# Performance work log

Hardware: AMD Instinct MI355X
Metric: run time of the kernel (lower is better)

Reference implementation:

```python
import jax, jax.numpy as jnp
import numpy as np

N_EMBED = 1024
HEAD_SIZE = 128

def setup_inputs() -> dict:
    key = jax.random.key(0)
    k1, k2, k3, k4 = jax.random.split(key, 4)
    x = jax.random.normal(k1, (8, 2048, N_EMBED), dtype=jnp.float32)
    # torch.nn.Linear default init: U(-1/sqrt(in), 1/sqrt(in)); stored as [out, in],
    # we store transposed [in, out] for x @ W.
    bound = 1.0 / np.sqrt(N_EMBED)
    Wk = jax.random.uniform(k2, (N_EMBED, HEAD_SIZE), jnp.float32, -bound, bound)
    Wq = jax.random.uniform(k3, (N_EMBED, HEAD_SIZE), jnp.float32, -bound, bound)
    Wv = jax.random.uniform(k4, (N_EMBED, HEAD_SIZE), jnp.float32, -bound, bound)
    return {"x": x, "Wk": Wk, "Wq": Wq, "Wv": Wv}

def reference(x, Wk, Wq, Wv):
    # x: [B, T, E]
    k = jnp.einsum('bte,eh->bth', x, Wk)  # [B, T, H]
    q = jnp.einsum('bte,eh->bth', x, Wq)
    v = jnp.einsum('bte,eh->bth', x, Wv)
    scale = 1.0 / np.sqrt(HEAD_SIZE).astype(np.float32)
    wei = jnp.einsum('bqh,bkh->bqk', q, k) * scale  # [B, T, T]
    wei = jax.nn.softmax(wei, axis=-1)
    out = jnp.einsum('bqk,bkh->bqh', wei, v)  # [B, T, H]
    return out
```

## Files before the change

kernel.cpp:

```cpp
#include <hip/hip_runtime.h>

#define BATCH 8
#define TLEN 2048
#define EMB 1024
#define HDIM 128
#define SCALE 0.08838834764831845f
#define NSPLIT 4

typedef _Float16 f16x8 __attribute__((ext_vector_type(8)));
typedef _Float16 f16x4 __attribute__((ext_vector_type(4)));
typedef float f32x4 __attribute__((ext_vector_type(4)));

static __device__ __forceinline__ f32x4 mfma16(f16x8 a, f16x8 b, f32x4 c) {
    return __builtin_amdgcn_mfma_f32_16x16x32_f16(a, b, c, 0, 0, 0);
}

__global__ void prep_w(const float* __restrict__ Wk, const float* __restrict__ Wq,
                       const float* __restrict__ Wv, _Float16* __restrict__ wtf) {
    int g = blockIdx.x * 256 + threadIdx.x;
    int lane = g & 63;
    int kstep = (g >> 6) & 31;
    int ntile = g >> 11;
    int n = ntile * 16 + (lane & 15);
    int sel = n >> 7;
    int h = n & 127;
    const float* W = (sel == 0) ? Wk : (sel == 1) ? Wq : Wv;
    int kbase = kstep * 32 + (lane >> 4) * 8;
    f16x8 o;
#pragma unroll
    for (int j = 0; j < 8; j++) {
        float v = W[(size_t)(kbase + j) * HDIM + h];
        if (sel == 1) v *= SCALE;
        o[j] = (_Float16)v;
    }
    *(f16x8*)&wtf[(size_t)g * 8] = o;
}

__global__ __launch_bounds__(256, 2) void proj_kernel(
        const float* __restrict__ x, const _Float16* __restrict__ wtf,
        _Float16* __restrict__ kb, _Float16* __restrict__ qb, _Float16* __restrict__ vbT) {
    __shared__ _Float16 xs[2][32 * 72];
    const int t = threadIdx.x;
    const int m0 = blockIdx.x * 32;
    const int wv = t >> 6;
    const int lane = t & 63;
    const int m16 = lane & 15;
    const int quad = lane >> 4;
    const int n0 = wv * 96;
    const int r0 = t >> 4;
    const int c0 = (t & 15) * 4;

    const f32x4 zero4 = {0.f, 0.f, 0.f, 0.f};
    f32x4 acc[2][6];
#pragma unroll
    for (int mt = 0; mt < 2; mt++)
#pragma unroll
        for (int nt = 0; nt < 6; nt++) acc[mt][nt] = zero4;

    const float* xrow0 = &x[(size_t)(m0 + r0) * EMB + c0];
    const float* xrow1 = &x[(size_t)(m0 + 16 + r0) * EMB + c0];

    float4 xv[2][2];
    f16x8 bf[2][12];
    xv[0][0] = *(const float4*)(xrow0);
    xv[0][1] = *(const float4*)(xrow1);
#pragma unroll
    for (int ks = 0; ks < 2; ks++)
#pragma unroll
        for (int nt = 0; nt < 6; nt++)
            bf[0][ks * 6 + nt] = *(const f16x8*)
                &wtf[((size_t)((wv * 6 + nt) * 32 + ks) * 64 + lane) * 8];

#pragma unroll
    for (int it = 0; it < 16; it++) {
        const int cur = it & 1, nxt = cur ^ 1;
#pragma unroll
        for (int i = 0; i < 2; i++) {
            f16x4 h;
            h[0] = (_Float16)xv[cur][i].x; h[1] = (_Float16)xv[cur][i].y;
            h[2] = (_Float16)xv[cur][i].z; h[3] = (_Float16)xv[cur][i].w;
            *(f16x4*)&xs[cur][(r0 + 16 * i) * 72 + c0] = h;
        }
        __syncthreads();
        if (it < 15) {
            xv[nxt][0] = *(const float4*)(xrow0 + (it + 1) * 64);
            xv[nxt][1] = *(const float4*)(xrow1 + (it + 1) * 64);
#pragma unroll
            for (int ks = 0; ks < 2; ks++)
#pragma unroll
                for (int nt = 0; nt < 6; nt++)
                    bf[nxt][ks * 6 + nt] = *(const f16x8*)
                        &wtf[((size_t)((wv * 6 + nt) * 32 + (it + 1) * 2 + ks) * 64 + lane) * 8];
        }
#pragma unroll
        for (int ks = 0; ks < 2; ks++) {
            f16x8 a0 = *(const f16x8*)&xs[cur][m16 * 72 + ks * 32 + quad * 8];
            f16x8 a1 = *(const f16x8*)&xs[cur][(16 + m16) * 72 + ks * 32 + quad * 8];
#pragma unroll
            for (int nt = 0; nt < 6; nt++) {
                acc[0][nt] = mfma16(a0, bf[cur][ks * 6 + nt], acc[0][nt]);
                acc[1][nt] = mfma16(a1, bf[cur][ks * 6 + nt], acc[1][nt]);
            }
        }
    }
#pragma unroll
    for (int nt = 0; nt < 6; nt++) {
        int n = n0 + nt * 16 + m16;
        int nsel = n >> 7;
        int h = n & 127;
        if (nsel < 2) {
            _Float16* dst = (nsel == 0) ? kb : qb;
#pragma unroll
            for (int mt = 0; mt < 2; mt++)
#pragma unroll
                for (int r = 0; r < 4; r++) {
                    int mg = m0 + mt * 16 + quad * 4 + r;
                    dst[(size_t)mg * HDIM + h] = (_Float16)acc[mt][nt][r];
                }
        } else {
#pragma unroll
            for (int mt = 0; mt < 2; mt++) {
                int mg = m0 + mt * 16 + quad * 4;
                int bb = mg >> 11, tok = mg & 2047;
                f16x4 pk;
#pragma unroll
                for (int r = 0; r < 4; r++) pk[r] = (_Float16)acc[mt][nt][r];
                *(f16x4*)&vbT[((size_t)bb * HDIM + h) * TLEN + tok] = pk;
            }
        }
    }
}

__global__ __launch_bounds__(256, 3) void attn_kernel(
        const _Float16* __restrict__ qb, const _Float16* __restrict__ kb,
        const _Float16* __restrict__ vbT,
        _Float16* __restrict__ po, float* __restrict__ pl) {
    __shared__ _Float16 kls[64 * 132];
    __shared__ _Float16 vtl[128 * 68];
    __shared__ _Float16 pls[4 * 32 * 72];
    const int t = threadIdx.x;
    const int qt = blockIdx.x;
    const int b = blockIdx.y;
    const int sp = blockIdx.z;
    const int wv = t >> 6;
    const int lane = t & 63;
    const int m16 = lane & 15;
    const int quad = lane >> 4;
    const int q0 = qt * 128 + wv * 32;
    _Float16* pw = pls + wv * (32 * 72);

    f16x8 qf[2][4];
#pragma unroll
    for (int mt = 0; mt < 2; mt++)
#pragma unroll
        for (int ks = 0; ks < 4; ks++)
            qf[mt][ks] = *(const f16x8*)
                &qb[((size_t)b * TLEN + q0 + mt * 16 + m16) * HDIM + ks * 32 + quad * 8];

    const f32x4 zero4 = {0.f, 0.f, 0.f, 0.f};
    f32x4 o[2][8];
    float lacc[2] = {0.f, 0.f};
#pragma unroll
    for (int mt = 0; mt < 2; mt++)
#pragma unroll
        for (int nt = 0; nt < 8; nt++) o[mt][nt] = zero4;

    for (int kt = sp * 8; kt < sp * 8 + 8; kt++) {
        const int k0 = kt * 64;
        f16x8 kreg[4];
#pragma unroll
        for (int rep = 0; rep < 4; rep++) {
            int u = t + rep * 256;
            kreg[rep] = *(const f16x8*)
                &kb[((size_t)b * TLEN + k0 + (u >> 4)) * HDIM + (u & 15) * 8];
        }
        __syncthreads();
#pragma unroll
        for (int rep = 0; rep < 4; rep++) {
            int u = t + rep * 256;
            *(f16x8*)&kls[(u >> 4) * 132 + (u & 15) * 8] = kreg[rep];
        }
#pragma unroll
        for (int rep = 0; rep < 4; rep++) {
            int u = t + rep * 256;
            f16x8 v = *(const f16x8*)
                &vbT[((size_t)b * HDIM + (u >> 3)) * TLEN + k0 + (u & 7) * 8];
            *(f16x8*)&vtl[(u >> 3) * 68 + (u & 7) * 8] = v;
        }
        __syncthreads();
#pragma unroll
        for (int kt_ = 0; kt_ < 4; kt_++) {
            f32x4 st0 = zero4, st1 = zero4;
#pragma unroll
            for (int ks = 0; ks < 4; ks++) {
                f16x8 kf = *(const f16x8*)&kls[(kt_ * 16 + m16) * 132 + ks * 32 + quad * 8];
                st0 = mfma16(kf, qf[0][ks], st0);
                st1 = mfma16(kf, qf[1][ks], st1);
            }
            f16x4 p0, p1;
#pragma unroll
            for (int r = 0; r < 4; r++) {
                float e0 = __expf(st0[r]);
                float e1 = __expf(st1[r]);
                lacc[0] += e0;
                lacc[1] += e1;
                p0[r] = (_Float16)e0;
                p1[r] = (_Float16)e1;
            }
            *(f16x4*)&pw[m16 * 72 + kt_ * 16 + quad * 4] = p0;
            *(f16x4*)&pw[(16 + m16) * 72 + kt_ * 16 + quad * 4] = p1;
        }
        f16x8 ap[2][2];
#pragma unroll
        for (int mt = 0; mt < 2; mt++)
#pragma unroll
            for (int kc = 0; kc < 2; kc++)
                ap[mt][kc] = *(const f16x8*)&pw[(mt * 16 + m16) * 72 + kc * 32 + quad * 8];
#pragma unroll
        for (int nt = 0; nt < 8; nt++) {
            f16x8 b0 = *(const f16x8*)&vtl[(nt * 16 + m16) * 68 + quad * 8];
            f16x8 b1 = *(const f16x8*)&vtl[(nt * 16 + m16) * 68 + 32 + quad * 8];
            o[0][nt] = mfma16(ap[0][0], b0, o[0][nt]);
            o[0][nt] = mfma16(ap[0][1], b1, o[0][nt]);
            o[1][nt] = mfma16(ap[1][0], b0, o[1][nt]);
            o[1][nt] = mfma16(ap[1][1], b1, o[1][nt]);
        }
    }
#pragma unroll
    for (int mt = 0; mt < 2; mt++) {
        lacc[mt] += __shfl_xor(lacc[mt], 16);
        lacc[mt] += __shfl_xor(lacc[mt], 32);
    }
#pragma unroll
    for (int mt = 0; mt < 2; mt++) {
        if (quad == 0)
            pl[((size_t)(sp * BATCH + b)) * TLEN + q0 + mt * 16 + m16] = lacc[mt];
#pragma unroll
        for (int r = 0; r < 4; r++) {
            int row = q0 + mt * 16 + quad * 4 + r;
            size_t prow = ((size_t)(sp * BATCH + b)) * TLEN + row;
#pragma unroll
            for (int nt = 0; nt < 8; nt++)
                po[prow * HDIM + nt * 16 + m16] = (_Float16)o[mt][nt][r];
        }
    }
}

__global__ void combine_kernel(const _Float16* __restrict__ po, const float* __restrict__ pl,
                               float* __restrict__ out) {
    int g = blockIdx.x * 256 + threadIdx.x;
    int row = g >> 5;
    int part = g & 31;
    int bb = row >> 11;
    int tok = row & 2047;
    float L = 0.f;
    float4 acc = {0.f, 0.f, 0.f, 0.f};
#pragma unroll
    for (int s = 0; s < NSPLIT; s++) {
        size_t prow = ((size_t)(s * BATCH + bb)) * TLEN + tok;
        L += pl[prow];
        f16x4 p = *(const f16x4*)&po[prow * HDIM + part * 4];
        acc.x += (float)p[0]; acc.y += (float)p[1];
        acc.z += (float)p[2]; acc.w += (float)p[3];
    }
    float inv = 1.f / L;
    float4 res = {acc.x * inv, acc.y * inv, acc.z * inv, acc.w * inv};
    *(float4*)&out[(size_t)row * HDIM + part * 4] = res;
}

extern "C" void kernel_launch(void* const* d_in, const int* in_sizes, int n_in,
                              void* d_out, int out_size, void* d_ws, size_t ws_size,
                              hipStream_t stream) {
    const float* x  = (const float*)d_in[0];
    const float* Wk = (const float*)d_in[1];
    const float* Wq = (const float*)d_in[2];
    const float* Wv = (const float*)d_in[3];
    float* out = (float*)d_out;
    char* ws = (char*)d_ws;
    _Float16* wtf = (_Float16*)(ws);
    _Float16* kb  = (_Float16*)(ws + (1ull << 20));
    _Float16* qb  = (_Float16*)(ws + (5ull << 20));
    _Float16* vbT = (_Float16*)(ws + (9ull << 20));
    _Float16* po  = (_Float16*)(ws + (13ull << 20));
    float* pl = (float*)(ws + (29ull << 20));

    prep_w<<<dim3(192), dim3(256), 0, stream>>>(Wk, Wq, Wv, wtf);
    proj_kernel<<<dim3(512), dim3(256), 0, stream>>>(x, wtf, kb, qb, vbT);
    attn_kernel<<<dim3(16, BATCH, NSPLIT), dim3(256), 0, stream>>>(qb, kb, vbT, po, pl);
    combine_kernel<<<dim3(2048), dim3(256), 0, stream>>>(po, pl, out);
}
```

Baseline: 157.7 us.

## Drop LDS staging in projection and attention, load operands directly from global

The projection kernel now uses 512-thread blocks covering 64 rows. Each wave reads its x fragments straight from global memory and converts them to fp16 in registers, removing the shared-memory staging and the barriers. The attention kernel likewise drops the K and V^T shared-memory tiles and the per-tile __syncthreads, reading MFMA operands directly from global memory through the cache; its launch bound goes from 3 to 2 blocks per CU. This removes LDS traffic and synchronisation, but adds redundant global/L2 loads (K/V tiles re-read by all four waves) and less latency hiding than the double-buffered path.

Result: slower. 225.3 us (+42.8%).

```diff
diff --git a/kernel.cpp b/kernel.cpp
--- a/kernel.cpp
+++ b/kernel.cpp
@@ -36,19 +36,18 @@
     *(f16x8*)&wtf[(size_t)g * 8] = o;
 }
 
-__global__ __launch_bounds__(256, 2) void proj_kernel(
+__global__ __launch_bounds__(512, 2) void proj_kernel(
         const float* __restrict__ x, const _Float16* __restrict__ wtf,
         _Float16* __restrict__ kb, _Float16* __restrict__ qb, _Float16* __restrict__ vbT) {
-    __shared__ _Float16 xs[2][32 * 72];
     const int t = threadIdx.x;
-    const int m0 = blockIdx.x * 32;
     const int wv = t >> 6;
     const int lane = t & 63;
     const int m16 = lane & 15;
     const int quad = lane >> 4;
-    const int n0 = wv * 96;
-    const int r0 = t >> 4;
-    const int c0 = (t & 15) * 4;
+    const int mhalf = (wv >> 2) * 32;
+    const int nq = wv & 3;
+    const int n0 = nq * 96;
+    const int m0 = blockIdx.x * 64;
 
     const f32x4 zero4 = {0.f, 0.f, 0.f, 0.f};
     f32x4 acc[2][6];
@@ -57,50 +56,35 @@
 #pragma unroll
         for (int nt = 0; nt < 6; nt++) acc[mt][nt] = zero4;
 
-    const float* xrow0 = &x[(size_t)(m0 + r0) * EMB + c0];
-    const float* xrow1 = &x[(size_t)(m0 + 16 + r0) * EMB + c0];
-
-    float4 xv[2][2];
-    f16x8 bf[2][12];
-    xv[0][0] = *(const float4*)(xrow0);
-    xv[0][1] = *(const float4*)(xrow1);
-#pragma unroll
-    for (int ks = 0; ks < 2; ks++)
+    const float* xr0 = &x[(size_t)(m0 + mhalf + m16) * EMB + quad * 8];
+    const float* xr1 = xr0 + 16 * EMB;
+    const _Float16* wq0 = &wtf[(size_t)(nq * 6) * 32 * 64 * 8 + (size_t)lane * 8];
+
+#pragma unroll 4
+    for (int kstep = 0; kstep < 32; kstep++) {
+        f16x8 af[2];
+        {
+            float4 lo0 = *(const float4*)(xr0 + kstep * 32);
+            float4 hi0 = *(const float4*)(xr0 + kstep * 32 + 4);
+            float4 lo1 = *(const float4*)(xr1 + kstep * 32);
+            float4 hi1 = *(const float4*)(xr1 + kstep * 32 + 4);
+            af[0][0] = (_Float16)lo0.x; af[0][1] = (_Float16)lo0.y;
+            af[0][2] = (_Float16)lo0.z; af[0][3] = (_Float16)lo0.w;
+            af[0][4] = (_Float16)hi0.x; af[0][5] = (_Float16)hi0.y;
+            af[0][6] = (_Float16)hi0.z; af[0][7] = (_Float16)hi0.w;
+            af[1][0] = (_Float16)lo1.x; af[1][1] = (_Float16)lo1.y;
+            af[1][2] = (_Float16)lo1.z; af[1][3] = (_Float16)lo1.w;
+            af[1][4] = (_Float16)hi1.x; af[1][5] = (_Float16)hi1.y;
+            af[1][6] = (_Float16)hi1.z; af[1][7] = (_Float16)hi1.w;
+        }
+        f16x8 bf[6];
 #pragma unroll
         for (int nt = 0; nt < 6; nt++)
-            bf[0][ks * 6 + nt] = *(const f16x8*)
-                &wtf[((size_t)((wv * 6 + nt) * 32 + ks) * 64 + lane) * 8];
-
-#pragma unroll
-    for (int it = 0; it < 16; it++) {
-        const int cur = it & 1, nxt = cur ^ 1;
-#pragma unroll
-        for (int i = 0; i < 2; i++) {
-            f16x4 h;
-            h[0] = (_Float16)xv[cur][i].x; h[1] = (_Float16)xv[cur][i].y;
-            h[2] = (_Float16)xv[cur][i].z; h[3] = (_Float16)xv[cur][i].w;
-            *(f16x4*)&xs[cur][(r0 + 16 * i) * 72 + c0] = h;
-        }
-        __syncthreads();
-        if (it < 15) {
-            xv[nxt][0] = *(const float4*)(xrow0 + (it + 1) * 64);
-            xv[nxt][1] = *(const float4*)(xrow1 + (it + 1) * 64);
-#pragma unroll
-            for (int ks = 0; ks < 2; ks++)
-#pragma unroll
-                for (int nt = 0; nt < 6; nt++)
-                    bf[nxt][ks * 6 + nt] = *(const f16x8*)
-                        &wtf[((size_t)((wv * 6 + nt) * 32 + (it + 1) * 2 + ks) * 64 + lane) * 8];
-        }
-#pragma unroll
-        for (int ks = 0; ks < 2; ks++) {
-            f16x8 a0 = *(const f16x8*)&xs[cur][m16 * 72 + ks * 32 + quad * 8];
-            f16x8 a1 = *(const f16x8*)&xs[cur][(16 + m16) * 72 + ks * 32 + quad * 8];
-#pragma unroll
-            for (int nt = 0; nt < 6; nt++) {
-                acc[0][nt] = mfma16(a0, bf[cur][ks * 6 + nt], acc[0][nt]);
-                acc[1][nt] = mfma16(a1, bf[cur][ks * 6 + nt], acc[1][nt]);
-            }
+            bf[nt] = *(const f16x8*)&wq0[(size_t)(nt * 32 + kstep) * 64 * 8];
+#pragma unroll
+        for (int nt = 0; nt < 6; nt++) {
+            acc[0][nt] = mfma16(af[0], bf[nt], acc[0][nt]);
+            acc[1][nt] = mfma16(af[1], bf[nt], acc[1][nt]);
         }
     }
 #pragma unroll
@@ -114,13 +98,13 @@
             for (int mt = 0; mt < 2; mt++)
 #pragma unroll
                 for (int r = 0; r < 4; r++) {
-                    int mg = m0 + mt * 16 + quad * 4 + r;
+                    int mg = m0 + mhalf + mt * 16 + quad * 4 + r;
                     dst[(size_t)mg * HDIM + h] = (_Float16)acc[mt][nt][r];
                 }
         } else {
 #pragma unroll
             for (int mt = 0; mt < 2; mt++) {
-                int mg = m0 + mt * 16 + quad * 4;
+                int mg = m0 + mhalf + mt * 16 + quad * 4;
                 int bb = mg >> 11, tok = mg & 2047;
                 f16x4 pk;
 #pragma unroll
@@ -131,12 +115,10 @@
     }
 }
 
-__global__ __launch_bounds__(256, 3) void attn_kernel(
+__global__ __launch_bounds__(256, 2) void attn_kernel(
         const _Float16* __restrict__ qb, const _Float16* __restrict__ kb,
         const _Float16* __restrict__ vbT,
         _Float16* __restrict__ po, float* __restrict__ pl) {
-    __shared__ _Float16 kls[64 * 132];
-    __shared__ _Float16 vtl[128 * 68];
     __shared__ _Float16 pls[4 * 32 * 72];
     const int t = threadIdx.x;
     const int qt = blockIdx.x;
@@ -165,35 +147,18 @@
 #pragma unroll
         for (int nt = 0; nt < 8; nt++) o[mt][nt] = zero4;
 
+    const _Float16* kbase = &kb[(size_t)b * TLEN * HDIM];
+    const _Float16* vbase = &vbT[(size_t)b * HDIM * TLEN];
+
     for (int kt = sp * 8; kt < sp * 8 + 8; kt++) {
         const int k0 = kt * 64;
-        f16x8 kreg[4];
-#pragma unroll
-        for (int rep = 0; rep < 4; rep++) {
-            int u = t + rep * 256;
-            kreg[rep] = *(const f16x8*)
-                &kb[((size_t)b * TLEN + k0 + (u >> 4)) * HDIM + (u & 15) * 8];
-        }
-        __syncthreads();
-#pragma unroll
-        for (int rep = 0; rep < 4; rep++) {
-            int u = t + rep * 256;
-            *(f16x8*)&kls[(u >> 4) * 132 + (u & 15) * 8] = kreg[rep];
-        }
-#pragma unroll
-        for (int rep = 0; rep < 4; rep++) {
-            int u = t + rep * 256;
-            f16x8 v = *(const f16x8*)
-                &vbT[((size_t)b * HDIM + (u >> 3)) * TLEN + k0 + (u & 7) * 8];
-            *(f16x8*)&vtl[(u >> 3) * 68 + (u & 7) * 8] = v;
-        }
-        __syncthreads();
 #pragma unroll
         for (int kt_ = 0; kt_ < 4; kt_++) {
             f32x4 st0 = zero4, st1 = zero4;
 #pragma unroll
             for (int ks = 0; ks < 4; ks++) {
-                f16x8 kf = *(const f16x8*)&kls[(kt_ * 16 + m16) * 132 + ks * 32 + quad * 8];
+                f16x8 kf = *(const f16x8*)
+                    &kbase[(size_t)(k0 + kt_ * 16 + m16) * HDIM + ks * 32 + quad * 8];
                 st0 = mfma16(kf, qf[0][ks], st0);
                 st1 = mfma16(kf, qf[1][ks], st1);
             }
@@ -218,8 +183,9 @@
                 ap[mt][kc] = *(const f16x8*)&pw[(mt * 16 + m16) * 72 + kc * 32 + quad * 8];
 #pragma unroll
         for (int nt = 0; nt < 8; nt++) {
-            f16x8 b0 = *(const f16x8*)&vtl[(nt * 16 + m16) * 68 + quad * 8];
-            f16x8 b1 = *(const f16x8*)&vtl[(nt * 16 + m16) * 68 + 32 + quad * 8];
+            const _Float16* vrow = &vbase[(size_t)(nt * 16 + m16) * TLEN + k0];
+            f16x8 b0 = *(const f16x8*)(vrow + quad * 8);
+            f16x8 b1 = *(const f16x8*)(vrow + 32 + quad * 8);
             o[0][nt] = mfma16(ap[0][0], b0, o[0][nt]);
             o[0][nt] = mfma16(ap[0][1], b1, o[0][nt]);
             o[1][nt] = mfma16(ap[1][0], b0, o[1][nt]);
@@ -285,7 +251,7 @@
     float* pl = (float*)(ws + (29ull << 20));
 
     prep_w<<<dim3(192), dim3(256), 0, stream>>>(Wk, Wq, Wv, wtf);
-    proj_kernel<<<dim3(512), dim3(256), 0, stream>>>(x, wtf, kb, qb, vbT);
+    proj_kernel<<<dim3(256), dim3(512), 0, stream>>>(x, wtf, kb, qb, vbT);
     attn_kernel<<<dim3(16, BATCH, NSPLIT), dim3(256), 0, stream>>>(qb, kb, vbT, po, pl);
     combine_kernel<<<dim3(2048), dim3(256), 0, stream>>>(po, pl, out);
 }
```

## Pre-convert x to fp16 MFMA-fragment layout and restructure projection kernel

Applied to the files above, without the earlier changes.

Adds a prep_x kernel that converts x from fp32 to fp16 and stores it in the per-lane MFMA fragment order, so the projection kernel loads A fragments straight from global memory without LDS staging or barriers. The projection kernel now runs 512 threads covering 64 rows per block, with two wave groups sharing the weight fragments. This removes in-loop conversion and __syncthreads, but adds a separate pass that writes and rereads a 32 MB fp16 copy of x, plus an extra kernel launch.

Measured after the change: 163.9 us. +3.9%, slower.

```diff
diff --git a/kernel.cpp b/kernel.cpp
--- a/kernel.cpp
+++ b/kernel.cpp
@@ -36,19 +36,49 @@
     *(f16x8*)&wtf[(size_t)g * 8] = o;
 }
 
-__global__ __launch_bounds__(256, 2) void proj_kernel(
-        const float* __restrict__ x, const _Float16* __restrict__ wtf,
+#define XPITCH 1048
+__global__ __launch_bounds__(256) void prep_x(const float* __restrict__ x,
+                                              _Float16* __restrict__ xf) {
+    __shared__ _Float16 ls[16 * XPITCH];
+    const int t = threadIdx.x;
+    const int mtile = blockIdx.x;
+    const float* src = x + (size_t)mtile * 16 * EMB;
+#pragma unroll
+    for (int i = 0; i < 16; i++) {
+        int f = t + i * 256;
+        int row = f >> 8;
+        int col = (f & 255) * 4;
+        float4 v = *(const float4*)&src[(size_t)row * EMB + col];
+        f16x4 h;
+        h[0] = (_Float16)v.x; h[1] = (_Float16)v.y;
+        h[2] = (_Float16)v.z; h[3] = (_Float16)v.w;
+        *(f16x4*)&ls[row * XPITCH + col] = h;
+    }
+    __syncthreads();
+    _Float16* dst = xf + (size_t)mtile * 32 * 512;
+#pragma unroll
+    for (int i = 0; i < 8; i++) {
+        int u = t + i * 256;
+        int kstep = u >> 6;
+        int lane = u & 63;
+        int kcol = kstep * 32 + (lane >> 4) * 8;
+        f16x8 v = *(const f16x8*)&ls[(lane & 15) * XPITCH + kcol];
+        *(f16x8*)&dst[(size_t)u * 8] = v;
+    }
+}
+
+__global__ __launch_bounds__(512, 2) void proj_kernel(
+        const _Float16* __restrict__ xf, const _Float16* __restrict__ wtf,
         _Float16* __restrict__ kb, _Float16* __restrict__ qb, _Float16* __restrict__ vbT) {
-    __shared__ _Float16 xs[2][32 * 72];
     const int t = threadIdx.x;
-    const int m0 = blockIdx.x * 32;
     const int wv = t >> 6;
     const int lane = t & 63;
     const int m16 = lane & 15;
     const int quad = lane >> 4;
-    const int n0 = wv * 96;
-    const int r0 = t >> 4;
-    const int c0 = (t & 15) * 4;
+    const int mhalf = (wv >> 2) * 32;
+    const int nq = wv & 3;
+    const int n0 = nq * 96;
+    const int m0 = blockIdx.x * 64;
 
     const f32x4 zero4 = {0.f, 0.f, 0.f, 0.f};
     f32x4 acc[2][6];
@@ -57,50 +87,24 @@
 #pragma unroll
         for (int nt = 0; nt < 6; nt++) acc[mt][nt] = zero4;
 
-    const float* xrow0 = &x[(size_t)(m0 + r0) * EMB + c0];
-    const float* xrow1 = &x[(size_t)(m0 + 16 + r0) * EMB + c0];
-
-    float4 xv[2][2];
-    f16x8 bf[2][12];
-    xv[0][0] = *(const float4*)(xrow0);
-    xv[0][1] = *(const float4*)(xrow1);
-#pragma unroll
-    for (int ks = 0; ks < 2; ks++)
+    const _Float16* xq = &xf[(size_t)(blockIdx.x * 4 + (wv >> 2) * 2) * 32 * 512
+                             + (size_t)lane * 8];
+    const _Float16* wq = &wtf[(size_t)(nq * 6) * 32 * 512 + (size_t)lane * 8];
+
+#pragma unroll 8
+    for (int kstep = 0; kstep < 32; kstep++) {
+        f16x8 af[2];
+#pragma unroll
+        for (int mt = 0; mt < 2; mt++)
+            af[mt] = *(const f16x8*)&xq[(size_t)(mt * 32 + kstep) * 512];
+        f16x8 bf[6];
 #pragma unroll
         for (int nt = 0; nt < 6; nt++)
-            bf[0][ks * 6 + nt] = *(const f16x8*)
-                &wtf[((size_t)((wv * 6 + nt) * 32 + ks) * 64 + lane) * 8];
-
-#pragma unroll
-    for (int it = 0; it < 16; it++) {
-        const int cur = it & 1, nxt = cur ^ 1;
-#pragma unroll
-        for (int i = 0; i < 2; i++) {
-            f16x4 h;
-            h[0] = (_Float16)xv[cur][i].x; h[1] = (_Float16)xv[cur][i].y;
-            h[2] = (_Float16)xv[cur][i].z; h[3] = (_Float16)xv[cur][i].w;
-            *(f16x4*)&xs[cur][(r0 + 16 * i) * 72 + c0] = h;
-        }
-        __syncthreads();
-        if (it < 15) {
-            xv[nxt][0] = *(const float4*)(xrow0 + (it + 1) * 64);
-            xv[nxt][1] = *(const float4*)(xrow1 + (it + 1) * 64);
-#pragma unroll
-            for (int ks = 0; ks < 2; ks++)
-#pragma unroll
-                for (int nt = 0; nt < 6; nt++)
-                    bf[nxt][ks * 6 + nt] = *(const f16x8*)
-                        &wtf[((size_t)((wv * 6 + nt) * 32 + (it + 1) * 2 + ks) * 64 + lane) * 8];
-        }
-#pragma unroll
-        for (int ks = 0; ks < 2; ks++) {
-            f16x8 a0 = *(const f16x8*)&xs[cur][m16 * 72 + ks * 32 + quad * 8];
-            f16x8 a1 = *(const f16x8*)&xs[cur][(16 + m16) * 72 + ks * 32 + quad * 8];
-#pragma unroll
-            for (int nt = 0; nt < 6; nt++) {
-                acc[0][nt] = mfma16(a0, bf[cur][ks * 6 + nt], acc[0][nt]);
-                acc[1][nt] = mfma16(a1, bf[cur][ks * 6 + nt], acc[1][nt]);
-            }
+            bf[nt] = *(const f16x8*)&wq[(size_t)(nt * 32 + kstep) * 512];
+#pragma unroll
+        for (int nt = 0; nt < 6; nt++) {
+            acc[0][nt] = mfma16(af[0], bf[nt], acc[0][nt]);
+            acc[1][nt] = mfma16(af[1], bf[nt], acc[1][nt]);
         }
     }
 #pragma unroll
@@ -114,13 +118,13 @@
             for (int mt = 0; mt < 2; mt++)
 #pragma unroll
                 for (int r = 0; r < 4; r++) {
-                    int mg = m0 + mt * 16 + quad * 4 + r;
+                    int mg = m0 + mhalf + mt * 16 + quad * 4 + r;
                     dst[(size_t)mg * HDIM + h] = (_Float16)acc[mt][nt][r];
                 }
         } else {
 #pragma unroll
             for (int mt = 0; mt < 2; mt++) {
-                int mg = m0 + mt * 16 + quad * 4;
+                int mg = m0 + mhalf + mt * 16 + quad * 4;
                 int bb = mg >> 11, tok = mg & 2047;
                 f16x4 pk;
 #pragma unroll
@@ -278,14 +282,16 @@
     float* out = (float*)d_out;
     char* ws = (char*)d_ws;
     _Float16* wtf = (_Float16*)(ws);
-    _Float16* kb  = (_Float16*)(ws + (1ull << 20));
-    _Float16* qb  = (_Float16*)(ws + (5ull << 20));
-    _Float16* vbT = (_Float16*)(ws + (9ull << 20));
-    _Float16* po  = (_Float16*)(ws + (13ull << 20));
-    float* pl = (float*)(ws + (29ull << 20));
+    _Float16* xf  = (_Float16*)(ws + (1ull << 20));
+    _Float16* kb  = (_Float16*)(ws + (33ull << 20));
+    _Float16* qb  = (_Float16*)(ws + (37ull << 20));
+    _Float16* vbT = (_Float16*)(ws + (41ull << 20));
+    _Float16* po  = (_Float16*)(ws + (45ull << 20));
+    float* pl = (float*)(ws + (61ull << 20));
 
     prep_w<<<dim3(192), dim3(256), 0, stream>>>(Wk, Wq, Wv, wtf);
-    proj_kernel<<<dim3(512), dim3(256), 0, stream>>>(x, wtf, kb, qb, vbT);
+    prep_x<<<dim3(1024), dim3(256), 0, stream>>>(x, xf);
+    proj_kernel<<<dim3(256), dim3(512), 0, stream>>>(xf, wtf, kb, qb, vbT);
     attn_kernel<<<dim3(16, BATCH, NSPLIT), dim3(256), 0, stream>>>(qb, kb, vbT, po, pl);
     combine_kernel<<<dim3(2048), dim3(256), 0, stream>>>(po, pl, out);
 }
```
